# Optimization experiments

Hardware: AMD Instinct MI355X
Metric: run time of the kernel (lower is better)

## Reference

```python
import jax, jax.numpy as jnp
import numpy as np

N_NODES = 25000
N_EDGES = 400000
N = 2          # per-node group dim (h.size(1))
IN_DIM = 64
HEADS = 4
HEAD_DIM = 16  # out_dim; HEADS*HEAD_DIM == IN_DIM here


def setup_inputs() -> dict:
    key = jax.random.key(0)
    ks = jax.random.split(key, 8)
    w_scale = 1.0 / np.sqrt(IN_DIM)
    return {
        "h": jax.random.normal(ks[0], (N_NODES, N, IN_DIM), jnp.float32),
        "e": jax.random.normal(ks[1], (N_EDGES, N, IN_DIM), jnp.float32),
        "W_Q": jax.random.normal(ks[2], (IN_DIM, HEADS * HEAD_DIM), jnp.float32) * w_scale,
        "W_K": jax.random.normal(ks[3], (IN_DIM, HEADS * HEAD_DIM), jnp.float32) * w_scale,
        "W_V": jax.random.normal(ks[4], (IN_DIM, HEADS * HEAD_DIM), jnp.float32) * w_scale,
        "W_repe": jax.random.normal(ks[5], (IN_DIM, HEADS * HEAD_DIM), jnp.float32) * w_scale,
        "src": jax.random.randint(ks[6], (N_EDGES,), 0, N_NODES, jnp.int32),
        "dst": jax.random.randint(ks[7], (N_EDGES,), 0, N_NODES, jnp.int32),
    }


def reference(h, e, W_Q, W_K, W_V, W_repe, src, dst):
    n_nodes, Nd, C = h.shape
    E = src.shape[0]
    # node-side projection Q_h: [n_nodes, N, H, D]
    Q_h = (h @ W_Q).reshape(n_nodes, Nd, HEADS, HEAD_DIM)
    # edge-side bias repe_e: [E, N, H, D]
    repe_e = (e @ W_repe).reshape(E, Nd, HEADS, HEAD_DIM)
    # compute_diff: relu(src - dst) on raw features  [E, N, C]
    diff = jax.nn.relu(h[src] - h[dst])
    k_diff = (diff @ W_K).reshape(E, Nd, HEADS, HEAD_DIM)
    v_diff = (diff @ W_V).reshape(E, Nd, HEADS, HEAD_DIM)
    # dst_cosim_diff: scale = ||k_diff|| * ||Q_h[dst]|| + 1e-6 (norm over last dim, keepdim)
    q_dst = Q_h[dst]  # [E, N, H, D]
    scale = (jnp.linalg.norm(k_diff, axis=-1, keepdims=True)
             * jnp.linalg.norm(q_dst, axis=-1, keepdims=True)) + 1e-6
    score = q_dst * k_diff * scale + repe_e
    msg = score * v_diff
    # update_all(copy_edge, max) -> segment max over dst; zero-degree nodes get 0 (DGL convention)
    h_out = jax.ops.segment_max(msg, dst, num_segments=n_nodes)
    h_out = jnp.where(jnp.isneginf(h_out), jnp.zeros((), h_out.dtype), h_out)
    return h_out
```

## Files before the change

### kernel.cpp

```cpp
#include <hip/hip_runtime.h>
#include <stdint.h>

#define N_NODES 25000
#define N_EDGES 400000
#define OUT_ELEMS 3200000
#define MAX_CHUNKS 72000

typedef __attribute__((ext_vector_type(8))) short short8;
typedef __attribute__((ext_vector_type(4))) float f32x4;

#define MFMA16(a, b, c) __builtin_amdgcn_mfma_f32_16x16x32_bf16((a), (b), (c), 0, 0, 0)

__device__ __forceinline__ short bf16r(float x) {
    unsigned u = __float_as_uint(x);
    u += 0x7FFFu + ((u >> 16) & 1u);
    return (short)(u >> 16);
}
__device__ __forceinline__ short bfr(float x) {
    return (short)((__float_as_uint(x) + 0x8000u) >> 16);
}

#define DPP_ADD(x, ctrl) \
    ((x) + __int_as_float(__builtin_amdgcn_update_dpp(0, __float_as_int(x), (ctrl), 0xF, 0xF, true)))
__device__ __forceinline__ float red16(float x) {
    x = DPP_ADD(x, 0xB1);
    x = DPP_ADD(x, 0x4E);
    x = DPP_ADD(x, 0x141);
    x = DPP_ADD(x, 0x140);
    return x;
}

__device__ __forceinline__ unsigned fmap(float x) {
    const unsigned u = __float_as_uint(x);
    return ((int)u >= 0) ? (u | 0x80000000u) : ~u;
}
#define MAPPED_NEG_INF 0x007FFFFFu

__device__ __forceinline__ short8 load_bfrag(const float* __restrict__ W,
                                             int colbase, int lane, int khalf) {
    const int n = colbase + (lane & 15);
    const int k0 = khalf * 32 + ((lane >> 4) << 3);
    short8 f;
    #pragma unroll
    for (int j = 0; j < 8; ++j) f[j] = bf16r(W[(k0 + j) * 64 + n]);
    return f;
}

__device__ __forceinline__ short8 afrag(const short* S, int lane, int khalf) {
    return *(const short8*)&S[(lane & 15) * 72 + khalf * 32 + ((lane >> 4) << 3)];
}

__global__ __launch_bounds__(256) void init_kernel(unsigned* __restrict__ out_u,
                                                   int* __restrict__ counts) {
    const int i = blockIdx.x * 256 + threadIdx.x;
    out_u[i] = MAPPED_NEG_INF;
    if (i < N_NODES) counts[i] = 0;
}

__global__ __launch_bounds__(256) void hist_kernel(const int* __restrict__ dst,
                                                   int* __restrict__ counts) {
    const int i = blockIdx.x * 256 + threadIdx.x;
    if (i < N_EDGES) atomicAdd(&counts[dst[i]], 1);
}

#define BPT 98
__global__ __launch_bounds__(256) void scan_kernel(const int* __restrict__ counts,
                                                   int* __restrict__ offsets,
                                                   int* __restrict__ cursor,
                                                   int* __restrict__ chunkoff) {
    __shared__ int pd[256];
    __shared__ int pc[256];
    const int t = threadIdx.x;
    const int base = t * BPT;
    int sd = 0, sc = 0;
    for (int j = 0; j < BPT; ++j) {
        const int idx = base + j;
        if (idx < N_NODES) {
            const int d = counts[idx];
            sd += d;
            sc += (d + 7) >> 3;
        }
    }
    pd[t] = sd; pc[t] = sc;
    __syncthreads();
    for (int d = 1; d < 256; d <<= 1) {
        const int ad = (t >= d) ? pd[t - d] : 0;
        const int ac = (t >= d) ? pc[t - d] : 0;
        __syncthreads();
        pd[t] += ad; pc[t] += ac;
        __syncthreads();
    }
    int rd = (t > 0) ? pd[t - 1] : 0;
    int rc = (t > 0) ? pc[t - 1] : 0;
    for (int j = 0; j < BPT; ++j) {
        const int idx = base + j;
        if (idx < N_NODES) {
            offsets[idx]  = rd;
            cursor[idx]   = rd;
            chunkoff[idx] = rc;
            const int d = counts[idx];
            rd += d;
            rc += (d + 7) >> 3;
        }
    }
    if (t == 255) { offsets[N_NODES] = pd[255]; chunkoff[N_NODES] = pc[255]; }
}

__global__ __launch_bounds__(256) void fill_kernel(const int* __restrict__ offsets,
                                                   const int* __restrict__ chunkoff,
                                                   int2* __restrict__ chunk_desc) {
    const int v = blockIdx.x * 256 + threadIdx.x;
    if (v < N_NODES) {
        const int off0 = offsets[v];
        const int deg  = offsets[v + 1] - off0;
        const int nch  = (deg + 7) >> 3;
        const int co   = chunkoff[v];
        for (int c = 0; c < nch; ++c) {
            int nval = deg - (c << 3);
            if (nval > 8) nval = 8;
            int2 d;
            d.x = v;
            d.y = (off0 + (c << 3)) | (nval << 24);
            chunk_desc[co + c] = d;
        }
    }
}

__global__ __launch_bounds__(256) void scatter_kernel(
    const int* __restrict__ src, const int* __restrict__ dst,
    int* __restrict__ cursor, int* __restrict__ perm, int* __restrict__ srcs) {
    const int i = blockIdx.x * 256 + threadIdx.x;
    if (i < N_EDGES) {
        const int d = dst[i];
        const int pos = atomicAdd(&cursor[d], 1);
        perm[pos] = i;
        srcs[pos] = src[i];
    }
}

__global__ __launch_bounds__(256) void q_mfma_kernel(
    const float* __restrict__ h, const float* __restrict__ Wq,
    const float* __restrict__ Wk, const float* __restrict__ Wv,
    const float* __restrict__ Wr, float* __restrict__ Q, short8* __restrict__ fw)
{
    __shared__ short sH[64 * 72];
    const int t = threadIdx.x;
    const int lane = t & 63, w = t >> 6;
    const int wcol = w << 4;
    const int ln = lane & 15, lq = lane >> 4;
    const int base = blockIdx.x * 64;

    const short8 b0 = load_bfrag(Wq, wcol, lane, 0);
    const short8 b1 = load_bfrag(Wq, wcol, lane, 1);

    {
        const int r = t >> 2, c4 = (t & 3) << 4;
        int row = base + r; if (row > 49999) row = 49999;
        const float4* p = (const float4*)&h[row * 64 + c4];
        short tmp[16];
        #pragma unroll
        for (int i = 0; i < 4; ++i) {
            float4 x = p[i];
            tmp[4*i+0] = bf16r(x.x); tmp[4*i+1] = bf16r(x.y);
            tmp[4*i+2] = bf16r(x.z); tmp[4*i+3] = bf16r(x.w);
        }
        *(short8*)&sH[r * 72 + c4]     = *(short8*)&tmp[0];
        *(short8*)&sH[r * 72 + c4 + 8] = *(short8*)&tmp[8];
    }
    __syncthreads();

    #pragma unroll
    for (int m = 0; m < 4; ++m) {
        const short* Sm = &sH[(m << 4) * 72];
        short8 a0 = afrag(Sm, lane, 0);
        short8 a1 = afrag(Sm, lane, 1);
        f32x4 acc = {0.f, 0.f, 0.f, 0.f};
        acc = MFMA16(a0, b0, acc);
        acc = MFMA16(a1, b1, acc);
        #pragma unroll
        for (int reg = 0; reg < 4; ++reg) {
            const int row = base + (m << 4) + (lq << 2) + reg;
            if (row < 50000) Q[row * 64 + wcol + ln] = acc[reg];
        }
    }

    if (blockIdx.x == 0) {
        fw[(w * 6 + 0) * 64 + lane] = load_bfrag(Wk, wcol, lane, 0);
        fw[(w * 6 + 1) * 64 + lane] = load_bfrag(Wk, wcol, lane, 1);
        fw[(w * 6 + 2) * 64 + lane] = load_bfrag(Wv, wcol, lane, 0);
        fw[(w * 6 + 3) * 64 + lane] = load_bfrag(Wv, wcol, lane, 1);
        fw[(w * 6 + 4) * 64 + lane] = load_bfrag(Wr, wcol, lane, 0);
        fw[(w * 6 + 5) * 64 + lane] = load_bfrag(Wr, wcol, lane, 1);
    }
}

__global__ __launch_bounds__(256, 4) void edge_chunk_kernel(
    const float* __restrict__ h, const float* __restrict__ e,
    const float* __restrict__ Q, const int* __restrict__ srcs,
    const int* __restrict__ perm, const int* __restrict__ chunkoff,
    const int2* __restrict__ chunk_desc, const short8* __restrict__ fw,
    unsigned* __restrict__ out_u)
{
    const int t = threadIdx.x;
    const int lane = t & 63;
    const int g = (blockIdx.x << 2) + (t >> 6);
    if (g >= chunkoff[N_NODES]) return;

    const int2 dsc = chunk_desc[g];
    const int v    = dsc.x;
    const int base = dsc.y & 0xFFFFFF;
    const int nval = dsc.y >> 24;

    const int ln = lane & 15, lq = lane >> 4;
    const int eloc = ln >> 1, nr = ln & 1;
    const int k0 = lq << 3;

    const int elc = (eloc < nval - 1) ? eloc : (nval - 1);
    const int ei  = base + elc;
    const int ed  = perm[ei];
    const int s   = srcs[ei];

    short8 bK0[4], bK1[4], bV0[4], bV1[4], bR0[4], bR1[4];
    #pragma unroll
    for (int hd = 0; hd < 4; ++hd) {
        bK0[hd] = fw[(hd * 6 + 0) * 64 + lane];
        bK1[hd] = fw[(hd * 6 + 1) * 64 + lane];
        bV0[hd] = fw[(hd * 6 + 2) * 64 + lane];
        bV1[hd] = fw[(hd * 6 + 3) * 64 + lane];
        bR0[hd] = fw[(hd * 6 + 4) * 64 + lane];
        bR1[hd] = fw[(hd * 6 + 5) * 64 + lane];
    }

    const float* __restrict__ hs  = &h[((s  << 1) + nr) << 6];
    const float* __restrict__ hdp = &h[((v  << 1) + nr) << 6];
    const float* __restrict__ ep  = &e[((ed << 1) + nr) << 6];

    short8 afr[2], gfr[2];
    #pragma unroll
    for (int half = 0; half < 2; ++half) {
        const int cb = (half << 5) + k0;
        const float4 s0 = *(const float4*)&hs[cb];
        const float4 s1 = *(const float4*)&hs[cb + 4];
        const float4 d0 = *(const float4*)&hdp[cb];
        const float4 d1 = *(const float4*)&hdp[cb + 4];
        const float4 e0 = *(const float4*)&ep[cb];
        const float4 e1 = *(const float4*)&ep[cb + 4];
        short8 ta, tg;
        ta[0] = bfr(fmaxf(s0.x - d0.x, 0.f));
        ta[1] = bfr(fmaxf(s0.y - d0.y, 0.f));
        ta[2] = bfr(fmaxf(s0.z - d0.z, 0.f));
        ta[3] = bfr(fmaxf(s0.w - d0.w, 0.f));
        ta[4] = bfr(fmaxf(s1.x - d1.x, 0.f));
        ta[5] = bfr(fmaxf(s1.y - d1.y, 0.f));
        ta[6] = bfr(fmaxf(s1.z - d1.z, 0.f));
        ta[7] = bfr(fmaxf(s1.w - d1.w, 0.f));
        tg[0] = bfr(e0.x); tg[1] = bfr(e0.y); tg[2] = bfr(e0.z); tg[3] = bfr(e0.w);
        tg[4] = bfr(e1.x); tg[5] = bfr(e1.y); tg[6] = bfr(e1.z); tg[7] = bfr(e1.w);
        afr[half] = ta;
        gfr[half] = tg;
    }

    float q0[4], q1[4], qn0[4], qn1[4];
    #pragma unroll
    for (int hd = 0; hd < 4; ++hd) {
        q0[hd] = Q[(v << 7) + (hd << 4) + ln];
        q1[hd] = Q[(v << 7) + 64 + (hd << 4) + ln];
        qn0[hd] = sqrtf(red16(q0[hd] * q0[hd]));
        qn1[hd] = sqrtf(red16(q1[hd] * q1[hd]));
    }

    const float NEG_INF = __uint_as_float(0xFF800000u);
    float rm0[4] = {NEG_INF, NEG_INF, NEG_INF, NEG_INF};
    float rm1[4] = {NEG_INF, NEG_INF, NEG_INF, NEG_INF};

    #pragma unroll
    for (int hd = 0; hd < 4; ++hd) {
        f32x4 aK = {0.f, 0.f, 0.f, 0.f}, aV = aK, aR = aK;
        aK = MFMA16(afr[0], bK0[hd], aK); aK = MFMA16(afr[1], bK1[hd], aK);
        aV = MFMA16(afr[0], bV0[hd], aV); aV = MFMA16(afr[1], bV1[hd], aV);
        aR = MFMA16(gfr[0], bR0[hd], aR); aR = MFMA16(gfr[1], bR1[hd], aR);

        #pragma unroll
        for (int reg = 0; reg < 4; ++reg) {
            const int rl = (lq << 2) + reg;
            const int el = rl >> 1;
            const int n2 = reg & 1;
            const bool valid = el < nval;
            const float kk = aK[reg];
            const float sk = red16(kk * kk);
            const float scale = sqrtf(sk) * (n2 ? qn1[hd] : qn0[hd]) + 1e-6f;
            const float qv = n2 ? q1[hd] : q0[hd];
            float msg = (qv * kk * scale + aR[reg]) * aV[reg];
            msg = valid ? msg : NEG_INF;
            if (n2) rm1[hd] = fmaxf(rm1[hd], msg);
            else    rm0[hd] = fmaxf(rm0[hd], msg);
        }
    }

    #pragma unroll
    for (int hd = 0; hd < 4; ++hd) {
        rm0[hd] = fmaxf(rm0[hd], __shfl_xor(rm0[hd], 16));
        rm0[hd] = fmaxf(rm0[hd], __shfl_xor(rm0[hd], 32));
        rm1[hd] = fmaxf(rm1[hd], __shfl_xor(rm1[hd], 16));
        rm1[hd] = fmaxf(rm1[hd], __shfl_xor(rm1[hd], 32));
    }
    const float o0 = (lq == 0) ? rm0[0] : (lq == 1) ? rm0[1] : (lq == 2) ? rm0[2] : rm0[3];
    const float o1 = (lq == 0) ? rm1[0] : (lq == 1) ? rm1[1] : (lq == 2) ? rm1[2] : rm1[3];
    atomicMax(&out_u[(v << 7) + lane],      fmap(o0));
    atomicMax(&out_u[(v << 7) + 64 + lane], fmap(o1));
}

__global__ __launch_bounds__(256) void final_kernel(unsigned* __restrict__ io) {
    const int i = blockIdx.x * 256 + threadIdx.x;
    uint4* p = (uint4*)io;
    uint4 m = p[i];
    unsigned a, b, c, d;
    a = (m.x & 0x80000000u) ? (m.x ^ 0x80000000u) : ~m.x;
    b = (m.y & 0x80000000u) ? (m.y ^ 0x80000000u) : ~m.y;
    c = (m.z & 0x80000000u) ? (m.z ^ 0x80000000u) : ~m.z;
    d = (m.w & 0x80000000u) ? (m.w ^ 0x80000000u) : ~m.w;
    if (a == 0xFF800000u) a = 0u;
    if (b == 0xFF800000u) b = 0u;
    if (c == 0xFF800000u) c = 0u;
    if (d == 0xFF800000u) d = 0u;
    m.x = a; m.y = b; m.z = c; m.w = d;
    p[i] = m;
}

extern "C" void kernel_launch(void* const* d_in, const int* in_sizes, int n_in,
                              void* d_out, int out_size, void* d_ws, size_t ws_size,
                              hipStream_t stream) {
    const float* h  = (const float*)d_in[0];
    const float* e  = (const float*)d_in[1];
    const float* Wq = (const float*)d_in[2];
    const float* Wk = (const float*)d_in[3];
    const float* Wv = (const float*)d_in[4];
    const float* Wr = (const float*)d_in[5];
    const int*   src = (const int*)d_in[6];
    const int*   dst = (const int*)d_in[7];
    float* out = (float*)d_out;

    float* Q        = (float*)d_ws;
    int*   counts   = (int*)d_ws + 3200000;
    int*   offsets  = (int*)d_ws + 3225000;
    int*   cursor   = (int*)d_ws + 3250008;
    int*   perm     = (int*)d_ws + 3275008;
    int*   srcs     = (int*)d_ws + 3675008;
    short8* fw      = (short8*)((int*)d_ws + 4075008);
    int*   chunkoff = (int*)d_ws + 4081152;
    int2*  chunk_desc = (int2*)((int*)d_ws + 4106154);

    init_kernel<<<12500, 256, 0, stream>>>((unsigned*)out, counts);
    hist_kernel<<<1563, 256, 0, stream>>>(dst, counts);
    scan_kernel<<<1, 256, 0, stream>>>(counts, offsets, cursor, chunkoff);
    fill_kernel<<<98, 256, 0, stream>>>(offsets, chunkoff, chunk_desc);
    scatter_kernel<<<1563, 256, 0, stream>>>(src, dst, cursor, perm, srcs);
    q_mfma_kernel<<<782, 256, 0, stream>>>(h, Wq, Wk, Wv, Wr, Q, fw);
    edge_chunk_kernel<<<17969, 256, 0, stream>>>(h, e, Q, srcs, perm,
                                                 chunkoff, chunk_desc, fw, (unsigned*)out);
    final_kernel<<<3125, 256, 0, stream>>>((unsigned*)out);
}
```

Measured before the change: 533.1 us.

## Precompute edge repe projection in CSR order and fold Q norm into Q

```diff
diff --git a/kernel.cpp b/kernel.cpp
--- a/kernel.cpp
+++ b/kernel.cpp
@@ -128,13 +128,15 @@
 
 __global__ __launch_bounds__(256) void scatter_kernel(
     const int* __restrict__ src, const int* __restrict__ dst,
-    int* __restrict__ cursor, int* __restrict__ perm, int* __restrict__ srcs) {
+    int* __restrict__ cursor, int* __restrict__ perm, int* __restrict__ srcs,
+    int* __restrict__ csr_pos) {
     const int i = blockIdx.x * 256 + threadIdx.x;
     if (i < N_EDGES) {
         const int d = dst[i];
         const int pos = atomicAdd(&cursor[d], 1);
         perm[pos] = i;
         srcs[pos] = src[i];
+        csr_pos[i] = pos;
     }
 }
 
@@ -179,8 +181,9 @@
         acc = MFMA16(a1, b1, acc);
         #pragma unroll
         for (int reg = 0; reg < 4; ++reg) {
+            const float qn = sqrtf(red16(acc[reg] * acc[reg]));
             const int row = base + (m << 4) + (lq << 2) + reg;
-            if (row < 50000) Q[row * 64 + wcol + ln] = acc[reg];
+            if (row < 50000) Q[row * 64 + wcol + ln] = acc[reg] * qn;
         }
     }
 
@@ -194,9 +197,167 @@
     }
 }
 
+__global__ __launch_bounds__(256) void repe_perm_kernel(
+    const float* __restrict__ e, const int* __restrict__ csr_pos,
+    const short8* __restrict__ fw, uint2* __restrict__ repe)
+{
+    const int t = threadIdx.x;
+    const int lane = t & 63;
+    const int g = (blockIdx.x << 2) + (t >> 6);
+    const int base8 = g << 3;
+    const int ln = lane & 15, lq = lane >> 4;
+    const int eloc = ln >> 1, nr = ln & 1;
+    const int k0 = lq << 3;
+
+    const float* __restrict__ ep = &e[((base8 + eloc) * 2 + nr) << 6];
+
+    short8 a0, a1;
+    #pragma unroll
+    for (int half = 0; half < 2; ++half) {
+        const int cb = (half << 5) + k0;
+        const float4 e0 = *(const float4*)&ep[cb];
+        const float4 e1 = *(const float4*)&ep[cb + 4];
+        short8 tg;
+        tg[0] = bfr(e0.x); tg[1] = bfr(e0.y); tg[2] = bfr(e0.z); tg[3] = bfr(e0.w);
+        tg[4] = bfr(e1.x); tg[5] = bfr(e1.y); tg[6] = bfr(e1.z); tg[7] = bfr(e1.w);
+        if (half == 0) a0 = tg; else a1 = tg;
+    }
+
+    const int p0 = csr_pos[base8 + (lq << 1)];
+    const int p1 = csr_pos[base8 + (lq << 1) + 1];
+
+    f32x4 aR[4];
+    #pragma unroll
+    for (int hd = 0; hd < 4; ++hd) {
+        f32x4 acc = {0.f, 0.f, 0.f, 0.f};
+        acc = MFMA16(a0, fw[(hd * 6 + 4) * 64 + lane], acc);
+        acc = MFMA16(a1, fw[(hd * 6 + 5) * 64 + lane], acc);
+        aR[hd] = acc;
+    }
+
+    #pragma unroll
+    for (int reg = 0; reg < 4; ++reg) {
+        const int p = (reg & 2) ? p1 : p0;
+        const int n = reg & 1;
+        uint2 pk;
+        pk.x = (unsigned)(unsigned short)bf16r(aR[0][reg])
+             | ((unsigned)(unsigned short)bf16r(aR[1][reg]) << 16);
+        pk.y = (unsigned)(unsigned short)bf16r(aR[2][reg])
+             | ((unsigned)(unsigned short)bf16r(aR[3][reg]) << 16);
+        repe[((p << 1) + n) * 16 + ln] = pk;
+    }
+}
+
+__global__ __launch_bounds__(256, 4) void edge_csr_kernel(
+    const float* __restrict__ h, const float* __restrict__ QQ,
+    const int* __restrict__ srcs, const int* __restrict__ chunkoff,
+    const int2* __restrict__ chunk_desc, const short8* __restrict__ fw,
+    const uint2* __restrict__ repe, unsigned* __restrict__ out_u)
+{
+    const int t = threadIdx.x;
+    const int lane = t & 63;
+    const int g = (blockIdx.x << 2) + (t >> 6);
+    if (g >= chunkoff[N_NODES]) return;
+
+    const int2 dsc = chunk_desc[g];
+    const int v    = dsc.x;
+    const int base = dsc.y & 0xFFFFFF;
+    const int nval = dsc.y >> 24;
+
+    const int ln = lane & 15, lq = lane >> 4;
+    const int eloc = ln >> 1, nr = ln & 1;
+    const int k0 = lq << 3;
+
+    const int elc = (eloc < nval - 1) ? eloc : (nval - 1);
+    const int s   = srcs[base + elc];
+
+    uint2 rp[4];
+    #pragma unroll
+    for (int reg = 0; reg < 4; ++reg) {
+        int el = (lq << 1) + ((reg & 2) >> 1);
+        if (el > nval - 1) el = nval - 1;
+        rp[reg] = repe[(((base + el) << 1) + (reg & 1)) * 16 + ln];
+    }
+
+    short8 bK0[4], bK1[4], bV0[4], bV1[4];
+    #pragma unroll
+    for (int hd = 0; hd < 4; ++hd) {
+        bK0[hd] = fw[(hd * 6 + 0) * 64 + lane];
+        bK1[hd] = fw[(hd * 6 + 1) * 64 + lane];
+        bV0[hd] = fw[(hd * 6 + 2) * 64 + lane];
+        bV1[hd] = fw[(hd * 6 + 3) * 64 + lane];
+    }
+
+    const float* __restrict__ hs  = &h[((s  << 1) + nr) << 6];
+    const float* __restrict__ hdp = &h[((v  << 1) + nr) << 6];
+
+    short8 afr[2];
+    #pragma unroll
+    for (int half = 0; half < 2; ++half) {
+        const int cb = (half << 5) + k0;
+        const float4 s0 = *(const float4*)&hs[cb];
+        const float4 s1 = *(const float4*)&hs[cb + 4];
+        const float4 d0 = *(const float4*)&hdp[cb];
+        const float4 d1 = *(const float4*)&hdp[cb + 4];
+        short8 ta;
+        ta[0] = bfr(fmaxf(s0.x - d0.x, 0.f));
+        ta[1] = bfr(fmaxf(s0.y - d0.y, 0.f));
+        ta[2] = bfr(fmaxf(s0.z - d0.z, 0.f));
+        ta[3] = bfr(fmaxf(s0.w - d0.w, 0.f));
+        ta[4] = bfr(fmaxf(s1.x - d1.x, 0.f));
+        ta[5] = bfr(fmaxf(s1.y - d1.y, 0.f));
+        ta[6] = bfr(fmaxf(s1.z - d1.z, 0.f));
+        ta[7] = bfr(fmaxf(s1.w - d1.w, 0.f));
+        afr[half] = ta;
+    }
+
+    float qq0[4], qq1[4];
+    #pragma unroll
+    for (int hd = 0; hd < 4; ++hd) {
+        qq0[hd] = QQ[(v << 7) + (hd << 4) + ln];
+        qq1[hd] = QQ[(v << 7) + 64 + (hd << 4) + ln];
+    }
+
+    const float NEG_INF = __uint_as_float(0xFF800000u);
+    float rm0[4] = {NEG_INF, NEG_INF, NEG_INF, NEG_INF};
+    float rm1[4] = {NEG_INF, NEG_INF, NEG_INF, NEG_INF};
+
+    #pragma unroll
+    for (int hd = 0; hd < 4; ++hd) {
+        f32x4 aK = {0.f, 0.f, 0.f, 0.f}, aV = aK;
+        aK = MFMA16(afr[0], bK0[hd], aK); aK = MFMA16(afr[1], bK1[hd], aK);
+        aV = MFMA16(afr[0], bV0[hd], aV); aV = MFMA16(afr[1], bV1[hd], aV);
+
+        #pragma unroll
+        for (int reg = 0; reg < 4; ++reg) {
+            const unsigned w32 = (hd < 2) ? rp[reg].x : rp[reg].y;
+            const float aRv = (hd & 1) ? __uint_as_float(w32 & 0xFFFF0000u)
+                                       : __uint_as_float(w32 << 16);
+            const float kk = aK[reg];
+            const float sk = red16(kk * kk);
+            const float qv = (reg & 1) ? qq1[hd] : qq0[hd];
+            const float msg = (qv * kk * sqrtf(sk) + aRv) * aV[reg];
+            if (reg & 1) rm1[hd] = fmaxf(rm1[hd], msg);
+            else         rm0[hd] = fmaxf(rm0[hd], msg);
+        }
+    }
+
+    #pragma unroll
+    for (int hd = 0; hd < 4; ++hd) {
+        rm0[hd] = fmaxf(rm0[hd], __shfl_xor(rm0[hd], 16));
+        rm0[hd] = fmaxf(rm0[hd], __shfl_xor(rm0[hd], 32));
+        rm1[hd] = fmaxf(rm1[hd], __shfl_xor(rm1[hd], 16));
+        rm1[hd] = fmaxf(rm1[hd], __shfl_xor(rm1[hd], 32));
+    }
+    const float o0 = (lq == 0) ? rm0[0] : (lq == 1) ? rm0[1] : (lq == 2) ? rm0[2] : rm0[3];
+    const float o1 = (lq == 0) ? rm1[0] : (lq == 1) ? rm1[1] : (lq == 2) ? rm1[2] : rm1[3];
+    atomicMax(&out_u[(v << 7) + lane],      fmap(o0));
+    atomicMax(&out_u[(v << 7) + 64 + lane], fmap(o1));
+}
+
 __global__ __launch_bounds__(256, 4) void edge_chunk_kernel(
     const float* __restrict__ h, const float* __restrict__ e,
-    const float* __restrict__ Q, const int* __restrict__ srcs,
+    const float* __restrict__ QQ, const int* __restrict__ srcs,
     const int* __restrict__ perm, const int* __restrict__ chunkoff,
     const int2* __restrict__ chunk_desc, const short8* __restrict__ fw,
     unsigned* __restrict__ out_u)
@@ -233,7 +394,7 @@
 
     const float* __restrict__ hs  = &h[((s  << 1) + nr) << 6];
     const float* __restrict__ hdp = &h[((v  << 1) + nr) << 6];
-    const float* __restrict__ ep  = &e[((ed << 1) + nr) << 6];
+    const float* __restrict__ ep  = &e[(((ed << 1) + nr) << 6)];
 
     short8 afr[2], gfr[2];
     #pragma unroll
@@ -260,13 +421,11 @@
         gfr[half] = tg;
     }
 
-    float q0[4], q1[4], qn0[4], qn1[4];
-    #pragma unroll
-    for (int hd = 0; hd < 4; ++hd) {
-        q0[hd] = Q[(v << 7) + (hd << 4) + ln];
-        q1[hd] = Q[(v << 7) + 64 + (hd << 4) + ln];
-        qn0[hd] = sqrtf(red16(q0[hd] * q0[hd]));
-        qn1[hd] = sqrtf(red16(q1[hd] * q1[hd]));
+    float qq0[4], qq1[4];
+    #pragma unroll
+    for (int hd = 0; hd < 4; ++hd) {
+        qq0[hd] = QQ[(v << 7) + (hd << 4) + ln];
+        qq1[hd] = QQ[(v << 7) + 64 + (hd << 4) + ln];
     }
 
     const float NEG_INF = __uint_as_float(0xFF800000u);
@@ -282,18 +441,12 @@
 
         #pragma unroll
         for (int reg = 0; reg < 4; ++reg) {
-            const int rl = (lq << 2) + reg;
-            const int el = rl >> 1;
-            const int n2 = reg & 1;
-            const bool valid = el < nval;
             const float kk = aK[reg];
             const float sk = red16(kk * kk);
-            const float scale = sqrtf(sk) * (n2 ? qn1[hd] : qn0[hd]) + 1e-6f;
-            const float qv = n2 ? q1[hd] : q0[hd];
-            float msg = (qv * kk * scale + aR[reg]) * aV[reg];
-            msg = valid ? msg : NEG_INF;
-            if (n2) rm1[hd] = fmaxf(rm1[hd], msg);
-            else    rm0[hd] = fmaxf(rm0[hd], msg);
+            const float qv = (reg & 1) ? qq1[hd] : qq0[hd];
+            const float msg = (qv * kk * sqrtf(sk) + aR[reg]) * aV[reg];
+            if (reg & 1) rm1[hd] = fmaxf(rm1[hd], msg);
+            else         rm0[hd] = fmaxf(rm0[hd], msg);
         }
     }
 
@@ -349,14 +502,23 @@
     short8* fw      = (short8*)((int*)d_ws + 4075008);
     int*   chunkoff = (int*)d_ws + 4081152;
     int2*  chunk_desc = (int2*)((int*)d_ws + 4106154);
+    int*   csr_pos  = (int*)d_ws + 4250154;
+    uint2* repe     = (uint2*)((int*)d_ws + 4650160);
+    const bool big_ws = ws_size >= 121002688ull;
 
     init_kernel<<<12500, 256, 0, stream>>>((unsigned*)out, counts);
     hist_kernel<<<1563, 256, 0, stream>>>(dst, counts);
     scan_kernel<<<1, 256, 0, stream>>>(counts, offsets, cursor, chunkoff);
     fill_kernel<<<98, 256, 0, stream>>>(offsets, chunkoff, chunk_desc);
-    scatter_kernel<<<1563, 256, 0, stream>>>(src, dst, cursor, perm, srcs);
+    scatter_kernel<<<1563, 256, 0, stream>>>(src, dst, cursor, perm, srcs, csr_pos);
     q_mfma_kernel<<<782, 256, 0, stream>>>(h, Wq, Wk, Wv, Wr, Q, fw);
-    edge_chunk_kernel<<<17969, 256, 0, stream>>>(h, e, Q, srcs, perm,
-                                                 chunkoff, chunk_desc, fw, (unsigned*)out);
+    if (big_ws) {
+        repe_perm_kernel<<<12500, 256, 0, stream>>>(e, csr_pos, fw, repe);
+        edge_csr_kernel<<<17969, 256, 0, stream>>>(h, Q, srcs, chunkoff,
+                                                   chunk_desc, fw, repe, (unsigned*)out);
+    } else {
+        edge_chunk_kernel<<<17969, 256, 0, stream>>>(h, e, Q, srcs, perm,
+                                                     chunkoff, chunk_desc, fw, (unsigned*)out);
+    }
     final_kernel<<<3125, 256, 0, stream>>>((unsigned*)out);
 }
```

After: 571.3 us. +7.2%, slower.
